# Kernel optimization log

Hardware: AMD Instinct MI355X
Metric: run time of the kernel (lower is better)

## Reference

```python
import jax, jax.numpy as jnp
import numpy as np

SIGMA = 5.0  # matches init_kwargs sigma


def so3_exp_map(w):
    """Rodrigues formula. w: [..., 3] axis-angle -> [..., 3, 3] rotation."""
    theta = jnp.sqrt(jnp.sum(w * w, axis=-1) + 1e-12)            # [...]
    wx, wy, wz = w[..., 0], w[..., 1], w[..., 2]
    z = jnp.zeros_like(wx)
    # normalized skew matrix K = hat(w) / theta
    K = jnp.stack([z, -wz, wy,
                   wz, z, -wx,
                   -wy, wx, z], axis=-1).reshape(w.shape[:-1] + (3, 3))
    K = K / theta[..., None, None]
    s = jnp.sin(theta)[..., None, None]
    c = (1.0 - jnp.cos(theta))[..., None, None]
    I = jnp.eye(3, dtype=w.dtype)
    return I + s * K + c * (K @ K)


def setup_inputs() -> dict:
    key = jax.random.key(0)
    k1, k2, k3, k4, k5 = jax.random.split(key, 5)
    P, N, E = 65536, 512, 4096
    # spread points/control points over a volume where sigma=5 is a meaningful scale
    points = jax.random.normal(k1, (P, 3), dtype=jnp.float32) * 10.0
    control_points = jax.random.normal(k2, (N, 3), dtype=jnp.float32) * 10.0
    rot_vec = jax.random.normal(k3, (N, 3), dtype=jnp.float32) * 0.1
    t = jax.random.normal(k4, (N, 3), dtype=jnp.float32) * 0.1
    edges = jax.random.randint(k5, (E, 2), 0, N, dtype=jnp.int64)
    return {"points": points, "control_points": control_points,
            "rot_vec": rot_vec, "t": t, "edges": edges}


def reference(points, control_points, rot_vec, t, edges):
    # ---- warp_points ----
    # local: [P, N, 3]
    local = points[:, None, :] - control_points[None, :, :]
    skin = jnp.exp(-jnp.sum(local * local, axis=-1) / (2.0 * SIGMA * SIGMA))  # [P, N]
    skin = skin / (jnp.sum(skin, axis=-1, keepdims=True) + 1e-5)
    R = so3_exp_map(rot_vec)                                    # [N, 3, 3]
    warped = (jnp.einsum('nij,pnj->pni', R, local)
              + t[None, :, :] + control_points[None, :, :])     # [P, N, 3]
    warped = jnp.sum(warped * skin[..., None], axis=1)          # [P, 3]
    # ---- reg_term ----
    i, j = edges[:, 0], edges[:, 1]
    ci, cj = control_points[i], control_points[j]               # [E, 3]
    ti, tj = t[i], t[j]
    Ri = R[i]                                                   # [E, 3, 3]
    resid = jnp.einsum('mij,mj->mi', Ri, cj - ci) + ci + ti - (cj + tj)
    reg = jnp.sum(resid * resid)
    return warped, reg
```

## Files before the change

### kernel.cpp

```cpp
#include <hip/hip_runtime.h>
#include <math.h>


constexpr int NP = 65536;
constexpr int PPB = 256;
constexpr float KEXP = -0.02f * 1.44269504088896340736f;
constexpr float M2K  = -2.0f * KEXP;
constexpr float WLOG = 10.0f;
constexpr float EPSS = 1e-5f * 1024.0f;

typedef _Float16 half8 __attribute__((ext_vector_type(8)));
typedef float    f32x4 __attribute__((ext_vector_type(4)));

__device__ __forceinline__ float fast_exp2(float x) {
    float r; asm("v_exp_f32 %0, %1" : "=v"(r) : "v"(x)); return r;
}

__device__ __forceinline__ void rodrigues(float wx, float wy, float wz, float* R) {
    float t2 = wx * wx + wy * wy + wz * wz + 1e-12f;
    float th = sqrtf(t2);
    float inv = 1.0f / th;
    float kx = wx * inv, ky = wy * inv, kz = wz * inv;
    float s = sinf(th);
    float c = 1.0f - cosf(th);
    float kxky = kx * ky, kxkz = kx * kz, kykz = ky * kz;
    R[0] = 1.0f - c * (ky * ky + kz * kz);
    R[1] = -s * kz + c * kxky;
    R[2] =  s * ky + c * kxkz;
    R[3] =  s * kz + c * kxky;
    R[4] = 1.0f - c * (kx * kx + kz * kz);
    R[5] = -s * kx + c * kykz;
    R[6] = -s * ky + c * kxkz;
    R[7] =  s * kx + c * kykz;
    R[8] = 1.0f - c * (kx * kx + ky * ky);
}

__global__ __launch_bounds__(512) void deform_kernel(
    const float* __restrict__ points,
    const float* __restrict__ cps,
    const float* __restrict__ rot,
    const float* __restrict__ tr,
    const int* __restrict__ edges,
    float* __restrict__ out)
{
    __shared__ float4 ndp[576];
    __shared__ half8 tf[16][64];
    __shared__ float cs[8][2][16][17];

    const int tid = threadIdx.x;
    const int bid = blockIdx.x;

    {
        const int n = tid;
        float R[9];
        rodrigues(rot[3 * n], rot[3 * n + 1], rot[3 * n + 2], R);
        float cx = cps[3 * n], cy = cps[3 * n + 1], cz = cps[3 * n + 2];
        float tx = tr[3 * n],  ty = tr[3 * n + 1],  tz = tr[3 * n + 2];
        float bx = tx + cx - (R[0] * cx + R[1] * cy + R[2] * cz);
        float by = ty + cy - (R[3] * cx + R[4] * cy + R[5] * cz);
        float bz = tz + cz - (R[6] * cx + R[7] * cy + R[8] * cz);
        ndp[n + (n >> 3)] = make_float4(M2K * cx, M2K * cy, M2K * cz,
                                        KEXP * (cx * cx + cy * cy + cz * cz) + WLOG);
        float tv[16] = {R[0], R[1], R[2], R[3], R[4], R[5], R[6], R[7], R[8],
                        bx, by, bz, 1.0f, 0.0f, 0.0f, 0.0f};
        const int ks = n >> 5, rr = n & 31, b = rr >> 3, j = rr & 7;
        #pragma unroll
        for (int c = 0; c < 16; ++c) {
            int cc = (c + n) & 15;
            ((_Float16*)&tf[ks][16 * b + cc])[j] = (_Float16)tv[cc];
        }
    }

    if (tid < 16) {
        const int e = bid * 16 + tid;
        const int i  = edges[2 * e + 0];
        const int j2 = edges[2 * e + 1];
        float Ri[9];
        rodrigues(rot[3 * i], rot[3 * i + 1], rot[3 * i + 2], Ri);
        float cix = cps[3 * i], ciy = cps[3 * i + 1], ciz = cps[3 * i + 2];
        float cjx = cps[3 * j2], cjy = cps[3 * j2 + 1], cjz = cps[3 * j2 + 2];
        float dx = cjx - cix, dy = cjy - ciy, dz = cjz - ciz;
        float rx = fmaf(Ri[0], dx, fmaf(Ri[1], dy, Ri[2] * dz)) + cix + tr[3 * i + 0] - cjx - tr[3 * j2 + 0];
        float ry = fmaf(Ri[3], dx, fmaf(Ri[4], dy, Ri[5] * dz)) + ciy + tr[3 * i + 1] - cjy - tr[3 * j2 + 1];
        float rz = fmaf(Ri[6], dx, fmaf(Ri[7], dy, Ri[8] * dz)) + ciz + tr[3 * i + 2] - cjz - tr[3 * j2 + 2];
        float acc = rx * rx + ry * ry + rz * rz;
        #pragma unroll
        for (int off = 8; off > 0; off >>= 1)
            acc += __shfl_down(acc, off, 16);
        if (tid == 0) atomicAdd(out + 3 * NP, acc);
    }

    __syncthreads();

    const int lane = tid & 63;
    const int wv   = tid >> 6;
    const int m    = lane & 15;
    const int bq   = lane >> 4;

    const int pA = bid * PPB + wv * 32 + m;
    const int pB = pA + 16;
    const float pxA = points[3 * pA], pyA = points[3 * pA + 1], pzA = points[3 * pA + 2];
    const float pxB = points[3 * pB], pyB = points[3 * pB + 1], pzB = points[3 * pB + 2];
    const float kpA = KEXP * (pxA * pxA + pyA * pyA + pzA * pzA);
    const float kpB = KEXP * (pxB * pxB + pyB * pyB + pzB * pzB);

    f32x4 acc0 = {0.0f, 0.0f, 0.0f, 0.0f};
    f32x4 acc1 = {0.0f, 0.0f, 0.0f, 0.0f};

    #pragma unroll 2
    for (int ks = 0; ks < 16; ++ks) {
        half8 bf = tf[ks][lane];
        const float4* cqp = &ndp[ks * 36 + bq * 9];
        float w0[8], w1[8];
        #pragma unroll
        for (int j = 0; j < 8; ++j) {
            float4 cq = cqp[j];
            w0[j] = fast_exp2(fmaf(cq.x, pxA, fmaf(cq.y, pyA, fmaf(cq.z, pzA, kpA + cq.w))));
            w1[j] = fast_exp2(fmaf(cq.x, pxB, fmaf(cq.y, pyB, fmaf(cq.z, pzB, kpB + cq.w))));
        }
        union { half8 v; unsigned int u[4]; } a0, a1;
        #pragma unroll
        for (int q = 0; q < 4; ++q) {
            a0.u[q] = __builtin_bit_cast(unsigned int,
                          __builtin_amdgcn_cvt_pkrtz(w0[2 * q], w0[2 * q + 1]));
            a1.u[q] = __builtin_bit_cast(unsigned int,
                          __builtin_amdgcn_cvt_pkrtz(w1[2 * q], w1[2 * q + 1]));
        }
        acc0 = __builtin_amdgcn_mfma_f32_16x16x32_f16(a0.v, bf, acc0, 0, 0, 0);
        acc1 = __builtin_amdgcn_mfma_f32_16x16x32_f16(a1.v, bf, acc1, 0, 0, 0);
    }

    #pragma unroll
    for (int jj = 0; jj < 4; ++jj) {
        cs[wv][0][bq * 4 + jj][m] = acc0[jj];
        cs[wv][1][bq * 4 + jj][m] = acc1[jj];
    }
    __syncthreads();

    if (tid < PPB) {
        const int p = bid * PPB + tid;
        const float* c = cs[tid >> 5][(tid >> 4) & 1][tid & 15];
        float px = points[3 * p], py = points[3 * p + 1], pz = points[3 * p + 2];
        float inv = 1.0f / (c[12] + EPSS);
        float ox = fmaf(c[0], px, fmaf(c[1], py, fmaf(c[2], pz, c[9])))  * inv;
        float oy = fmaf(c[3], px, fmaf(c[4], py, fmaf(c[5], pz, c[10]))) * inv;
        float oz = fmaf(c[6], px, fmaf(c[7], py, fmaf(c[8], pz, c[11]))) * inv;
        out[3 * p + 0] = ox;
        out[3 * p + 1] = oy;
        out[3 * p + 2] = oz;
    }
}

extern "C" void kernel_launch(void* const* d_in, const int* in_sizes, int n_in,
                              void* d_out, int out_size, void* d_ws, size_t ws_size,
                              hipStream_t stream) {
    const float* points = (const float*)d_in[0];
    const float* cps    = (const float*)d_in[1];
    const float* rot    = (const float*)d_in[2];
    const float* tr     = (const float*)d_in[3];
    const int*   edges  = (const int*)d_in[4];
    float* out = (float*)d_out;
    deform_kernel<<<NP / PPB, 512, 0, stream>>>(points, cps, rot, tr, edges, out);
}
```

Measured before the change: 75.32 us.

## Halve block threads, give each wave four point tiles, use hardware sin/cos

Each block now runs 256 threads (4 waves) instead of 512. Each wave handles 64 points as four 16-point MFMA tiles, so the control-point constants loaded from LDS are reused across four tiles. The per-block Rodrigues setup for 512 control points is split two per thread, and sinf/cosf are replaced by v_sin/v_cos hardware instructions on angle/2π to cut transcendental cost. The risks are lower occupancy from fewer waves per block and launch_bounds(256,1), higher register pressure, and setup work per thread that doubles.

```diff
diff --git a/kernel.cpp b/kernel.cpp
--- a/kernel.cpp
+++ b/kernel.cpp
@@ -8,6 +8,7 @@
 constexpr float M2K  = -2.0f * KEXP;
 constexpr float WLOG = 10.0f;
 constexpr float EPSS = 1e-5f * 1024.0f;
+constexpr float INV2PI = 0.15915494309189535f;
 
 typedef _Float16 half8 __attribute__((ext_vector_type(8)));
 typedef float    f32x4 __attribute__((ext_vector_type(4)));
@@ -15,14 +16,21 @@
 __device__ __forceinline__ float fast_exp2(float x) {
     float r; asm("v_exp_f32 %0, %1" : "=v"(r) : "v"(x)); return r;
 }
+__device__ __forceinline__ float fast_sin2pi(float x) {
+    float r; asm("v_sin_f32 %0, %1" : "=v"(r) : "v"(x)); return r;
+}
+__device__ __forceinline__ float fast_cos2pi(float x) {
+    float r; asm("v_cos_f32 %0, %1" : "=v"(r) : "v"(x)); return r;
+}
 
 __device__ __forceinline__ void rodrigues(float wx, float wy, float wz, float* R) {
     float t2 = wx * wx + wy * wy + wz * wz + 1e-12f;
     float th = sqrtf(t2);
     float inv = 1.0f / th;
     float kx = wx * inv, ky = wy * inv, kz = wz * inv;
-    float s = sinf(th);
-    float c = 1.0f - cosf(th);
+    float rev = th * INV2PI;
+    float s = fast_sin2pi(rev);
+    float c = 1.0f - fast_cos2pi(rev);
     float kxky = kx * ky, kxkz = kx * kz, kykz = ky * kz;
     R[0] = 1.0f - c * (ky * ky + kz * kz);
     R[1] = -s * kz + c * kxky;
@@ -35,7 +43,7 @@
     R[8] = 1.0f - c * (kx * kx + ky * ky);
 }
 
-__global__ __launch_bounds__(512) void deform_kernel(
+__global__ __launch_bounds__(256, 1) void deform_kernel(
     const float* __restrict__ points,
     const float* __restrict__ cps,
     const float* __restrict__ rot,
@@ -45,13 +53,13 @@
 {
     __shared__ float4 ndp[576];
     __shared__ half8 tf[16][64];
-    __shared__ float cs[8][2][16][17];
+    __shared__ float cs[4][4][16][17];
 
     const int tid = threadIdx.x;
     const int bid = blockIdx.x;
 
-    {
-        const int n = tid;
+    #pragma unroll
+    for (int n = tid; n < 512; n += 256) {
         float R[9];
         rodrigues(rot[3 * n], rot[3 * n + 1], rot[3 * n + 2], R);
         float cx = cps[3 * n], cy = cps[3 * n + 1], cz = cps[3 * n + 2];
@@ -97,54 +105,59 @@
     const int m    = lane & 15;
     const int bq   = lane >> 4;
 
-    const int pA = bid * PPB + wv * 32 + m;
-    const int pB = pA + 16;
-    const float pxA = points[3 * pA], pyA = points[3 * pA + 1], pzA = points[3 * pA + 2];
-    const float pxB = points[3 * pB], pyB = points[3 * pB + 1], pzB = points[3 * pB + 2];
-    const float kpA = KEXP * (pxA * pxA + pyA * pyA + pzA * pzA);
-    const float kpB = KEXP * (pxB * pxB + pyB * pyB + pzB * pzB);
+    const int pbase = bid * PPB + wv * 64 + m;
+    float px[4], py[4], pz[4], kp2[4];
+    #pragma unroll
+    for (int t = 0; t < 4; ++t) {
+        int p = pbase + t * 16;
+        px[t] = points[3 * p];
+        py[t] = points[3 * p + 1];
+        pz[t] = points[3 * p + 2];
+        kp2[t] = KEXP * (px[t] * px[t] + py[t] * py[t] + pz[t] * pz[t]);
+    }
 
-    f32x4 acc0 = {0.0f, 0.0f, 0.0f, 0.0f};
-    f32x4 acc1 = {0.0f, 0.0f, 0.0f, 0.0f};
+    f32x4 acc[4] = {{0,0,0,0}, {0,0,0,0}, {0,0,0,0}, {0,0,0,0}};
 
     #pragma unroll 2
     for (int ks = 0; ks < 16; ++ks) {
         half8 bf = tf[ks][lane];
         const float4* cqp = &ndp[ks * 36 + bq * 9];
-        float w0[8], w1[8];
+        float4 cq[8];
         #pragma unroll
-        for (int j = 0; j < 8; ++j) {
-            float4 cq = cqp[j];
-            w0[j] = fast_exp2(fmaf(cq.x, pxA, fmaf(cq.y, pyA, fmaf(cq.z, pzA, kpA + cq.w))));
-            w1[j] = fast_exp2(fmaf(cq.x, pxB, fmaf(cq.y, pyB, fmaf(cq.z, pzB, kpB + cq.w))));
+        for (int j = 0; j < 8; ++j) cq[j] = cqp[j];
+
+        #pragma unroll
+        for (int t = 0; t < 4; ++t) {
+            float w[8];
+            #pragma unroll
+            for (int j = 0; j < 8; ++j)
+                w[j] = fast_exp2(fmaf(cq[j].x, px[t],
+                                 fmaf(cq[j].y, py[t],
+                                 fmaf(cq[j].z, pz[t], kp2[t] + cq[j].w))));
+            union { half8 v; unsigned int u[4]; } a;
+            #pragma unroll
+            for (int q = 0; q < 4; ++q)
+                a.u[q] = __builtin_bit_cast(unsigned int,
+                             __builtin_amdgcn_cvt_pkrtz(w[2 * q], w[2 * q + 1]));
+            acc[t] = __builtin_amdgcn_mfma_f32_16x16x32_f16(a.v, bf, acc[t], 0, 0, 0);
         }
-        union { half8 v; unsigned int u[4]; } a0, a1;
-        #pragma unroll
-        for (int q = 0; q < 4; ++q) {
-            a0.u[q] = __builtin_bit_cast(unsigned int,
-                          __builtin_amdgcn_cvt_pkrtz(w0[2 * q], w0[2 * q + 1]));
-            a1.u[q] = __builtin_bit_cast(unsigned int,
-                          __builtin_amdgcn_cvt_pkrtz(w1[2 * q], w1[2 * q + 1]));
-        }
-        acc0 = __builtin_amdgcn_mfma_f32_16x16x32_f16(a0.v, bf, acc0, 0, 0, 0);
-        acc1 = __builtin_amdgcn_mfma_f32_16x16x32_f16(a1.v, bf, acc1, 0, 0, 0);
     }
 
     #pragma unroll
-    for (int jj = 0; jj < 4; ++jj) {
-        cs[wv][0][bq * 4 + jj][m] = acc0[jj];
-        cs[wv][1][bq * 4 + jj][m] = acc1[jj];
-    }
+    for (int t = 0; t < 4; ++t)
+        #pragma unroll
+        for (int jj = 0; jj < 4; ++jj)
+            cs[wv][t][bq * 4 + jj][m] = acc[t][jj];
     __syncthreads();
 
-    if (tid < PPB) {
+    {
         const int p = bid * PPB + tid;
-        const float* c = cs[tid >> 5][(tid >> 4) & 1][tid & 15];
-        float px = points[3 * p], py = points[3 * p + 1], pz = points[3 * p + 2];
+        const float* c = cs[tid >> 6][(tid >> 4) & 3][tid & 15];
+        float qx = points[3 * p], qy = points[3 * p + 1], qz = points[3 * p + 2];
         float inv = 1.0f / (c[12] + EPSS);
-        float ox = fmaf(c[0], px, fmaf(c[1], py, fmaf(c[2], pz, c[9])))  * inv;
-        float oy = fmaf(c[3], px, fmaf(c[4], py, fmaf(c[5], pz, c[10]))) * inv;
-        float oz = fmaf(c[6], px, fmaf(c[7], py, fmaf(c[8], pz, c[11]))) * inv;
+        float ox = fmaf(c[0], qx, fmaf(c[1], qy, fmaf(c[2], qz, c[9])))  * inv;
+        float oy = fmaf(c[3], qx, fmaf(c[4], qy, fmaf(c[5], qz, c[10]))) * inv;
+        float oz = fmaf(c[6], qx, fmaf(c[7], qy, fmaf(c[8], qz, c[11]))) * inv;
         out[3 * p + 0] = ox;
         out[3 * p + 1] = oy;
         out[3 * p + 2] = oz;
@@ -160,5 +173,5 @@
     const float* tr     = (const float*)d_in[3];
     const int*   edges  = (const int*)d_in[4];
     float* out = (float*)d_out;
-    deform_kernel<<<NP / PPB, 512, 0, stream>>>(points, cps, rot, tr, edges, out);
+    deform_kernel<<<NP / PPB, 256, 0, stream>>>(points, cps, rot, tr, edges, out);
 }
```

Result: slower. 77.86 us (+3.4%).
